# Kernel optimization log

Measured on AMD Instinct MI355X. Metric: run time of the kernel, lower is better.

## Reference

```python
import jax, jax.numpy as jnp
import numpy as np

EPS = 1e-8

def rms_norm(x, scale):
    # full RMSNorm over last dim (p < 0 branch): norm/sqrt(d)
    d = x.shape[-1]
    norm = jnp.linalg.norm(x, ord=2, axis=-1, keepdims=True)
    rms = norm * (d ** -0.5)
    return scale * (x / (rms + EPS))

def setup_inputs() -> dict:
    key = jax.random.key(0)
    ks = jax.random.split(key, 4)
    B, N, C, H = 2, 2048, 1024, 16
    hd = C // H
    x = jax.random.normal(ks[0], (B, N, C), dtype=jnp.float32)
    Wqkv = jax.random.normal(ks[1], (C, 3 * C), dtype=jnp.float32) * (C ** -0.5)
    Wproj = jax.random.normal(ks[2], (C, C), dtype=jnp.float32) * (C ** -0.5)
    bproj = jnp.zeros((C,), dtype=jnp.float32)
    q_scale = jnp.ones((hd,), dtype=jnp.float32)
    k_scale = jnp.ones((hd,), dtype=jnp.float32)
    return {"x": x, "Wqkv": Wqkv, "Wproj": Wproj, "bproj": bproj,
            "q_scale": q_scale, "k_scale": k_scale}

def reference(x, Wqkv, Wproj, bproj, q_scale, k_scale):
    B, N, C = x.shape
    H = 16
    hd = C // H
    scale = hd ** -0.5
    qkv = (x @ Wqkv).reshape(B, N, 3, H, hd)
    qkv = jnp.transpose(qkv, (2, 0, 3, 1, 4))  # t b h n c
    q, k, v = qkv[0], qkv[1], qkv[2]
    q = rms_norm(q, q_scale)
    k = rms_norm(k, k_scale)
    attn = jnp.einsum('bhnc,bhmc->bhnm', q, k) * scale
    attn = jax.nn.softmax(attn, axis=-1)
    out = jnp.einsum('bhnm,bhmc->bhnc', attn, v)
    out = jnp.transpose(out, (0, 2, 1, 3)).reshape(B, N, C)
    return out @ Wproj + bproj
```

## Files before the change

kernel.cpp:

```cpp
#include <hip/hip_runtime.h>


typedef _Float16 half_t;
typedef __attribute__((ext_vector_type(2))) __fp16 fp16x2;
typedef __attribute__((ext_vector_type(4))) _Float16 half4v;
typedef __attribute__((ext_vector_type(8))) _Float16 half8;
typedef __attribute__((ext_vector_type(4))) float f32x4;
typedef __attribute__((ext_vector_type(4))) unsigned uint4v;

#define DI __device__ __forceinline__

DI void gl_lds16(const void* g, void* l) {
    __builtin_amdgcn_global_load_lds((const __attribute__((address_space(1))) void*)g,
                                     (__attribute__((address_space(3))) void*)l, 16, 0, 0);
}

DI float exp2_fast(float x) {
    float r;
    asm("v_exp_f32 %0, %1" : "=v"(r) : "v"(x));
    return r;
}

DI void pl32_swap(unsigned& a, unsigned& b) {
    asm("v_permlane32_swap_b32 %0, %1" : "+v"(a), "+v"(b));
}
DI void pl16_swap(unsigned& a, unsigned& b) {
    asm("v_permlane16_swap_b32 %0, %1" : "+v"(a), "+v"(b));
}

DI unsigned pk_u32(float lo, float hi) {
    fp16x2 t = __builtin_amdgcn_cvt_pkrtz(lo, hi);
    return *(unsigned*)&t;
}

__global__ void prep_all(const float* __restrict__ x, const float* __restrict__ Wqkv,
                         const float* __restrict__ Wproj, half_t* __restrict__ xh,
                         half_t* __restrict__ wqt, half_t* __restrict__ wpt) {
    __shared__ float t[32][33];
    int bid = blockIdx.x;
    if (bid < 4096) {
        int i = (bid * 256 + threadIdx.x) * 4;
        float4 v = *(const float4*)(x + i);
        half4v o;
        o[0] = (half_t)v.x; o[1] = (half_t)v.y; o[2] = (half_t)v.z; o[3] = (half_t)v.w;
        *(half4v*)(xh + i) = o;
    } else if (bid < 4096 + 3072) {
        int i = bid - 4096;
        int c0 = (i % 96) * 32, r0 = (i / 96) * 32;
        int tx = threadIdx.x & 31, ty = threadIdx.x >> 5;
#pragma unroll
        for (int k = 0; k < 4; k++)
            t[ty + 8 * k][tx] = Wqkv[(size_t)(r0 + ty + 8 * k) * 3072 + c0 + tx];
        __syncthreads();
#pragma unroll
        for (int k = 0; k < 4; k++)
            wqt[(size_t)(c0 + ty + 8 * k) * 1024 + r0 + tx] = (half_t)t[tx][ty + 8 * k];
    } else {
        int i = bid - 4096 - 3072;
        int c0 = (i % 32) * 32, r0 = (i / 32) * 32;
        int tx = threadIdx.x & 31, ty = threadIdx.x >> 5;
#pragma unroll
        for (int k = 0; k < 4; k++)
            t[ty + 8 * k][tx] = Wproj[(size_t)(r0 + ty + 8 * k) * 1024 + c0 + tx];
        __syncthreads();
#pragma unroll
        for (int k = 0; k < 4; k++)
            wpt[(size_t)(c0 + ty + 8 * k) * 1024 + r0 + tx] = (half_t)t[tx][ty + 8 * k];
    }
}

__global__ __launch_bounds__(256) void gemm_qkv(
    const half_t* __restrict__ A, const half_t* __restrict__ Bt,
    const float* __restrict__ qs, const float* __restrict__ ks,
    half_t* __restrict__ qh, half_t* __restrict__ kh, half_t* __restrict__ vth) {
    const int K = 1024;
    __shared__ __align__(16) half_t Al[2][128 * 64];
    __shared__ __align__(16) half_t Bl[2][128 * 64];
    int tid = threadIdx.x;
    int w = tid >> 6, l = tid & 63;
    int wr = w >> 1, wc = w & 1;
    int g = l >> 4, r = l & 15;
    int m0 = blockIdx.x * 128, n0 = blockIdx.y * 128;
    f32x4 acc[4][4] = {};

#define STAGE_QKV(kt, buf)                                                        \
    {                                                                             \
        _Pragma("unroll")                                                         \
        for (int p = 0; p < 4; p++) {                                             \
            int ci = p * 256 + tid;                                               \
            int row = ci >> 3, c = ci & 7, lc = c ^ (row & 7);                    \
            gl_lds16(A + (size_t)(m0 + row) * K + (kt) * 64 + lc * 8,             \
                     &Al[buf][0] + ci * 8);                                       \
            gl_lds16(Bt + (size_t)(n0 + row) * K + (kt) * 64 + lc * 8,            \
                     &Bl[buf][0] + ci * 8);                                       \
        }                                                                         \
    }

    STAGE_QKV(0, 0);
    __syncthreads();
    int cur = 0;
    for (int kt = 0; kt < 16; kt++) {
        if (kt < 15) STAGE_QKV(kt + 1, cur ^ 1);
#pragma unroll
        for (int ks2 = 0; ks2 < 2; ks2++) {
            half8 af[4], bf[4];
#pragma unroll
            for (int i = 0; i < 4; i++) {
                int row = wr * 64 + i * 16 + r;
                af[i] = *(const half8*)(&Al[cur][0] + row * 64 + (((4 * ks2 + g) ^ (row & 7)) << 3));
                int rowb = wc * 64 + i * 16 + r;
                bf[i] = *(const half8*)(&Bl[cur][0] + rowb * 64 + (((4 * ks2 + g) ^ (rowb & 7)) << 3));
            }
#pragma unroll
            for (int i = 0; i < 4; i++)
#pragma unroll
                for (int j = 0; j < 4; j++)
                    acc[i][j] = __builtin_amdgcn_mfma_f32_16x16x32_f16(af[i], bf[j], acc[i][j], 0, 0, 0);
        }
        __syncthreads();
        cur ^= 1;
    }

    int tsec = n0 >> 10;
    if (tsec == 2) {
#pragma unroll
        for (int i = 0; i < 4; i++)
#pragma unroll
            for (int j = 0; j < 4; j++) {
                int gcol = n0 + wc * 64 + j * 16 + r;
                int h = (gcol >> 6) & 15;
                int f = gcol & 63;
                int growb = m0 + wr * 64 + i * 16 + g * 4;
                int b = growb >> 11;
                int n = growb & 2047;
                half4v pv;
#pragma unroll
                for (int rr = 0; rr < 4; rr++) pv[rr] = (half_t)acc[i][j][rr];
                *(half4v*)(vth + ((size_t)(b * 16 + h) * 64 + f) * 2048 + n) = pv;
            }
    } else {
        const float* sc = (tsec == 0) ? qs : ks;
        half_t* dst = (tsec == 0) ? qh : kh;
        float extra = (tsec == 0) ? (0.125f * 1.44269504f) : 1.0f;
        float scv[4];
#pragma unroll
        for (int j = 0; j < 4; j++) scv[j] = sc[j * 16 + r];
#pragma unroll
        for (int i = 0; i < 4; i++)
#pragma unroll
            for (int rr = 0; rr < 4; rr++) {
                float ss = 0.f;
#pragma unroll
                for (int j = 0; j < 4; j++) ss += acc[i][j][rr] * acc[i][j][rr];
#pragma unroll
                for (int d = 1; d < 16; d <<= 1) ss += __shfl_xor(ss, d, 64);
                float inv = extra / (sqrtf(ss) * 0.125f + 1e-8f);
                int grow = m0 + wr * 64 + i * 16 + g * 4 + rr;
                int b = grow >> 11;
                int n = grow & 2047;
#pragma unroll
                for (int j = 0; j < 4; j++) {
                    int gcol = n0 + wc * 64 + j * 16 + r;
                    int h = (gcol >> 6) & 15;
                    int f = gcol & 63;
                    dst[((size_t)(b * 16 + h) * 2048 + n) * 64 + f] =
                        (half_t)(acc[i][j][rr] * inv * scv[j]);
                }
            }
    }
}

__global__ __launch_bounds__(512, 6) void attn(
    const half_t* __restrict__ qh, const half_t* __restrict__ kh,
    const half_t* __restrict__ vth, half_t* __restrict__ aoh) {
    int bh = blockIdx.y;
    int q0 = blockIdx.x * 128;
    const half_t* Qp = qh + (size_t)bh * 2048 * 64;
    const half_t* Kp = kh + (size_t)bh * 2048 * 64;
    const half_t* Vp = vth + (size_t)bh * 64 * 2048;
    __shared__ __align__(16) half_t Kl[2][64 * 64];
    __shared__ __align__(16) half_t Vl[2][64 * 64];
    int tid = threadIdx.x, w = tid >> 6, l = tid & 63, g = l >> 4, r = l & 15;

    int srow = tid >> 3, sc = tid & 7, slc = sc ^ (srow & 7);
    const half_t* kst = Kp + (size_t)srow * 64 + slc * 8;
    const half_t* vst = Vp + (size_t)srow * 2048 + slc * 8;

    int koff[8], voff[8];
#pragma unroll
    for (int ks = 0; ks < 2; ks++)
#pragma unroll
        for (int tt = 0; tt < 4; tt++) {
            int row = tt * 16 + r;
            koff[ks * 4 + tt] = row * 64 + (((4 * ks + g) ^ (row & 7)) << 3);
        }
#pragma unroll
    for (int ks2 = 0; ks2 < 2; ks2++)
#pragma unroll
        for (int cf = 0; cf < 4; cf++) {
            int row = cf * 16 + r;
            voff[ks2 * 4 + cf] = row * 64 + (((4 * ks2 + g) ^ (row & 7)) << 3);
        }

    half8 qf[2];
#pragma unroll
    for (int ks = 0; ks < 2; ks++)
        qf[ks] = *(const half8*)(Qp + (size_t)(q0 + w * 16 + r) * 64 + ks * 32 + g * 8);

    f32x4 o[4] = {};
    float m = -1e30f, lsum = 0.f;

    gl_lds16(kst, &Kl[0][0] + tid * 8);
    gl_lds16(vst, &Vl[0][0] + tid * 8);
    __syncthreads();

#define ATTN_TILE(BUF, T)                                                          \
    {                                                                              \
        if ((T) < 31) {                                                            \
            gl_lds16(kst + ((T) + 1) * 4096, &Kl[(BUF) ^ 1][0] + tid * 8);         \
            gl_lds16(vst + ((T) + 1) * 64, &Vl[(BUF) ^ 1][0] + tid * 8);           \
        }                                                                          \
        const half_t* Kc = &Kl[BUF][0];                                            \
        const half_t* Vc = &Vl[BUF][0];                                            \
        f32x4 s[4] = {};                                                           \
        _Pragma("unroll")                                                          \
        for (int ks = 0; ks < 2; ks++)                                             \
            _Pragma("unroll")                                                      \
            for (int tt = 0; tt < 4; tt++) {                                       \
                half8 kf = *(const half8*)(Kc + koff[ks * 4 + tt]);                \
                s[tt] = __builtin_amdgcn_mfma_f32_16x16x32_f16(kf, qf[ks], s[tt], 0, 0, 0); \
            }                                                                      \
        float thr = m + 11.0f;                                                     \
        bool ok = true;                                                            \
        _Pragma("unroll")                                                          \
        for (int tt = 0; tt < 4; tt++)                                             \
            _Pragma("unroll")                                                      \
            for (int e = 0; e < 4; e++) ok = ok && (s[tt][e] <= thr);              \
        if (!__all(ok)) {                                                          \
            float mx = -1e30f;                                                     \
            _Pragma("unroll")                                                      \
            for (int tt = 0; tt < 4; tt++)                                         \
                mx = fmaxf(mx, fmaxf(fmaxf(s[tt][0], s[tt][1]), fmaxf(s[tt][2], s[tt][3]))); \
            mx = fmaxf(mx, __shfl_xor(mx, 16, 64));                                \
            mx = fmaxf(mx, __shfl_xor(mx, 32, 64));                                \
            float mn = fmaxf(m, mx);                                               \
            float fac = exp2_fast(m - mn);                                         \
            lsum *= fac;                                                           \
            _Pragma("unroll")                                                      \
            for (int cf = 0; cf < 4; cf++) {                                       \
                o[cf][0] *= fac; o[cf][1] *= fac; o[cf][2] *= fac; o[cf][3] *= fac; \
            }                                                                      \
            m = mn;                                                                \
        }                                                                          \
        _Pragma("unroll")                                                          \
        for (int tt = 0; tt < 4; tt++)                                             \
            _Pragma("unroll")                                                      \
            for (int e = 0; e < 4; e++) {                                          \
                float p = exp2_fast(s[tt][e] - m);                                 \
                s[tt][e] = p;                                                      \
                lsum += p;                                                         \
            }                                                                      \
        unsigned W[4][2];                                                          \
        _Pragma("unroll")                                                          \
        for (int tt = 0; tt < 4; tt++) {                                           \
            W[tt][0] = pk_u32(s[tt][0], s[tt][1]);                                 \
            W[tt][1] = pk_u32(s[tt][2], s[tt][3]);                                 \
        }                                                                          \
        _Pragma("unroll")                                                          \
        for (int ks2 = 0; ks2 < 2; ks2++) {                                        \
            unsigned b0 = W[2 * ks2][0], b2 = W[2 * ks2 + 1][0];                   \
            unsigned b1 = W[2 * ks2][1], b3 = W[2 * ks2 + 1][1];                   \
            pl32_swap(b0, b2); pl16_swap(b0, b2);                                  \
            pl32_swap(b1, b3); pl16_swap(b1, b3);                                  \
            uint4v pw; pw[0] = b0; pw[1] = b1; pw[2] = b2; pw[3] = b3;             \
            half8 pf = *(half8*)&pw;                                               \
            _Pragma("unroll")                                                      \
            for (int cf = 0; cf < 4; cf++) {                                       \
                half8 vf = *(const half8*)(Vc + voff[ks2 * 4 + cf]);               \
                o[cf] = __builtin_amdgcn_mfma_f32_16x16x32_f16(vf, pf, o[cf], 0, 0, 0); \
            }                                                                      \
        }                                                                          \
        __syncthreads();                                                           \
    }

    for (int t = 0; t < 32; t += 2) {
        ATTN_TILE(0, t);
        ATTN_TILE(1, t + 1);
    }

    lsum += __shfl_xor(lsum, 16, 64);
    lsum += __shfl_xor(lsum, 32, 64);

    int b = bh >> 4, h = bh & 15;
    int n = q0 + w * 16 + r;
    float inv = 1.0f / lsum;
#pragma unroll
    for (int cf = 0; cf < 4; cf++) {
        half4v ov;
#pragma unroll
        for (int reg = 0; reg < 4; reg++) ov[reg] = (half_t)(o[cf][reg] * inv);
        *(half4v*)(aoh + ((size_t)b * 2048 + n) * 1024 + h * 64 + cf * 16 + g * 4) = ov;
    }
}

__global__ __launch_bounds__(256) void gemm_proj(
    const half_t* __restrict__ A, const half_t* __restrict__ Bt,
    const float* __restrict__ bias, float* __restrict__ out) {
    const int K = 1024;
    __shared__ __align__(16) half_t Al[128 * 64];
    __shared__ __align__(16) half_t Bl[128 * 64];
    int tid = threadIdx.x, w = tid >> 6, l = tid & 63;
    int wr = w >> 1, wc = w & 1, g = l >> 4, r = l & 15;
    int m0 = blockIdx.x * 128, n0 = blockIdx.y * 128;
    f32x4 acc[4][4] = {};

    for (int k0 = 0; k0 < K; k0 += 64) {
#pragma unroll
        for (int p = 0; p < 4; p++) {
            int ci = (p * 4 + w) * 64 + l;
            int row = ci >> 3, c = ci & 7;
            int lc = c ^ (row & 7);
            gl_lds16(A + (size_t)(m0 + row) * K + k0 + lc * 8, Al + (p * 4 + w) * 512);
            gl_lds16(Bt + (size_t)(n0 + row) * K + k0 + lc * 8, Bl + (p * 4 + w) * 512);
        }
        __syncthreads();
#pragma unroll
        for (int ks = 0; ks < 2; ks++) {
            half8 af[4], bf[4];
#pragma unroll
            for (int i = 0; i < 4; i++) {
                int row = wr * 64 + i * 16 + r;
                af[i] = *(const half8*)(Al + row * 64 + (((4 * ks + g) ^ (row & 7)) << 3));
                int rowb = wc * 64 + i * 16 + r;
                bf[i] = *(const half8*)(Bl + rowb * 64 + (((4 * ks + g) ^ (rowb & 7)) << 3));
            }
#pragma unroll
            for (int i = 0; i < 4; i++)
#pragma unroll
                for (int j = 0; j < 4; j++)
                    acc[i][j] = __builtin_amdgcn_mfma_f32_16x16x32_f16(af[i], bf[j], acc[i][j], 0, 0, 0);
        }
        __syncthreads();
    }

#pragma unroll
    for (int i = 0; i < 4; i++)
#pragma unroll
        for (int j = 0; j < 4; j++) {
            int gcol = n0 + wc * 64 + j * 16 + r;
            float bv = bias[gcol];
#pragma unroll
            for (int rr = 0; rr < 4; rr++) {
                int grow = m0 + wr * 64 + i * 16 + g * 4 + rr;
                out[(size_t)grow * 1024 + gcol] = acc[i][j][rr] + bv;
            }
        }
}

extern "C" void kernel_launch(void* const* d_in, const int* in_sizes, int n_in,
                              void* d_out, int out_size, void* d_ws, size_t ws_size,
                              hipStream_t stream) {
    const float* x = (const float*)d_in[0];
    const float* Wqkv = (const float*)d_in[1];
    const float* Wproj = (const float*)d_in[2];
    const float* bproj = (const float*)d_in[3];
    const float* qscale = (const float*)d_in[4];
    const float* kscale = (const float*)d_in[5];
    float* out = (float*)d_out;

    char* ws = (char*)d_ws;
    half_t* xh  = (half_t*)(ws + 0);
    half_t* wqt = (half_t*)(ws + 8388608);
    half_t* wpt = (half_t*)(ws + 14680064);
    half_t* qh  = (half_t*)(ws + 16777216);
    half_t* kh  = (half_t*)(ws + 25165824);
    half_t* vth = (half_t*)(ws + 33554432);
    half_t* aoh = (half_t*)(ws + 41943040);

    prep_all<<<8192, 256, 0, stream>>>(x, Wqkv, Wproj, xh, wqt, wpt);
    gemm_qkv<<<dim3(32, 24), 256, 0, stream>>>(xh, wqt, qscale, kscale, qh, kh, vth);
    attn<<<dim3(16, 32), 512, 0, stream>>>(qh, kh, vth, aoh);
    gemm_proj<<<dim3(32, 8), 256, 0, stream>>>(aoh, wpt, bproj, out);
}
```

Measured before the change: 131.6 us.

## Split attention over key dimension into two halves with a combine kernel

Splits each attention block's 2048-key loop into two independent halves via a third grid dimension, doubling the grid from 512 to 1024 blocks to improve occupancy across the GPU's compute units. Each half writes a normalized fp16 partial output plus its running max and sum, and a new combine kernel merges them with exp2-weighted rescaling. This adds an extra kernel launch and an extra round trip of partial outputs through memory, and stores intermediate results in fp16. Workspace buffers are rearranged so the partials reuse the region that held the converted input and QKV weights.

```diff
diff --git a/kernel.cpp b/kernel.cpp
--- a/kernel.cpp
+++ b/kernel.cpp
@@ -170,14 +170,15 @@
     }
 }
 
-__global__ __launch_bounds__(512, 6) void attn(
+__global__ __launch_bounds__(512, 8) void attn(
     const half_t* __restrict__ qh, const half_t* __restrict__ kh,
-    const half_t* __restrict__ vth, half_t* __restrict__ aoh) {
-    int bh = blockIdx.y;
+    const half_t* __restrict__ vth, half_t* __restrict__ po16,
+    float2* __restrict__ pml) {
+    int bh = blockIdx.y, hf = blockIdx.z;
     int q0 = blockIdx.x * 128;
     const half_t* Qp = qh + (size_t)bh * 2048 * 64;
-    const half_t* Kp = kh + (size_t)bh * 2048 * 64;
-    const half_t* Vp = vth + (size_t)bh * 64 * 2048;
+    const half_t* Kp = kh + (size_t)bh * 2048 * 64 + (size_t)hf * 1024 * 64;
+    const half_t* Vp = vth + (size_t)bh * 64 * 2048 + hf * 1024;
     __shared__ __align__(16) half_t Kl[2][64 * 64];
     __shared__ __align__(16) half_t Vl[2][64 * 64];
     int tid = threadIdx.x, w = tid >> 6, l = tid & 63, g = l >> 4, r = l & 15;
@@ -216,7 +217,7 @@
 
 #define ATTN_TILE(BUF, T)                                                          \
     {                                                                              \
-        if ((T) < 31) {                                                            \
+        if ((T) < 15) {                                                            \
             gl_lds16(kst + ((T) + 1) * 4096, &Kl[(BUF) ^ 1][0] + tid * 8);         \
             gl_lds16(vst + ((T) + 1) * 64, &Vl[(BUF) ^ 1][0] + tid * 8);           \
         }                                                                          \
@@ -283,7 +284,7 @@
         __syncthreads();                                                           \
     }
 
-    for (int t = 0; t < 32; t += 2) {
+    for (int t = 0; t < 16; t += 2) {
         ATTN_TILE(0, t);
         ATTN_TILE(1, t + 1);
     }
@@ -291,16 +292,40 @@
     lsum += __shfl_xor(lsum, 16, 64);
     lsum += __shfl_xor(lsum, 32, 64);
 
-    int b = bh >> 4, h = bh & 15;
     int n = q0 + w * 16 + r;
+    size_t pq = (size_t)(hf * 32 + bh) * 2048 + n;
     float inv = 1.0f / lsum;
 #pragma unroll
     for (int cf = 0; cf < 4; cf++) {
         half4v ov;
 #pragma unroll
         for (int reg = 0; reg < 4; reg++) ov[reg] = (half_t)(o[cf][reg] * inv);
-        *(half4v*)(aoh + ((size_t)b * 2048 + n) * 1024 + h * 64 + cf * 16 + g * 4) = ov;
-    }
+        *(half4v*)(po16 + pq * 64 + cf * 16 + g * 4) = ov;
+    }
+    if (l < 16) pml[pq] = make_float2(m, lsum);
+}
+
+__global__ void attn_combine(const half_t* __restrict__ po16,
+                             const float2* __restrict__ pml,
+                             half_t* __restrict__ aoh) {
+    int idx = blockIdx.x * 256 + threadIdx.x;
+    int d4 = idx & 15;
+    int q = (idx >> 4) & 2047;
+    int bh = idx >> 15;
+    float2 ml0 = pml[(size_t)bh * 2048 + q];
+    float2 ml1 = pml[(size_t)(32 + bh) * 2048 + q];
+    float M = fmaxf(ml0.x, ml1.x);
+    float w0 = exp2_fast(ml0.x - M) * ml0.y;
+    float w1 = exp2_fast(ml1.x - M) * ml1.y;
+    float inv = 1.0f / (w0 + w1);
+    w0 *= inv; w1 *= inv;
+    half4v a = *(const half4v*)(po16 + ((size_t)bh * 2048 + q) * 64 + d4 * 4);
+    half4v b2 = *(const half4v*)(po16 + ((size_t)(32 + bh) * 2048 + q) * 64 + d4 * 4);
+    half4v o;
+#pragma unroll
+    for (int e = 0; e < 4; e++) o[e] = (half_t)((float)a[e] * w0 + (float)b2[e] * w1);
+    int b = bh >> 4, h = bh & 15;
+    *(half4v*)(aoh + ((size_t)b * 2048 + q) * 1024 + h * 64 + d4 * 4) = o;
 }
 
 __global__ __launch_bounds__(256) void gemm_proj(
@@ -369,16 +394,19 @@
     float* out = (float*)d_out;
 
     char* ws = (char*)d_ws;
-    half_t* xh  = (half_t*)(ws + 0);
-    half_t* wqt = (half_t*)(ws + 8388608);
-    half_t* wpt = (half_t*)(ws + 14680064);
-    half_t* qh  = (half_t*)(ws + 16777216);
-    half_t* kh  = (half_t*)(ws + 25165824);
-    half_t* vth = (half_t*)(ws + 33554432);
-    half_t* aoh = (half_t*)(ws + 41943040);
+    half_t* xh   = (half_t*)(ws + 0);
+    half_t* wqt  = (half_t*)(ws + 8388608);
+    half_t* po16 = (half_t*)(ws + 0);
+    float2* pml  = (float2*)(ws + 16777216);
+    half_t* qh   = (half_t*)(ws + 17825792);
+    half_t* kh   = (half_t*)(ws + 26214400);
+    half_t* vth  = (half_t*)(ws + 34603008);
+    half_t* wpt  = (half_t*)(ws + 42991616);
+    half_t* aoh  = (half_t*)(ws + 45088768);
 
     prep_all<<<8192, 256, 0, stream>>>(x, Wqkv, Wproj, xh, wqt, wpt);
     gemm_qkv<<<dim3(32, 24), 256, 0, stream>>>(xh, wqt, qscale, kscale, qh, kh, vth);
-    attn<<<dim3(16, 32), 512, 0, stream>>>(qh, kh, vth, aoh);
+    attn<<<dim3(16, 32, 2), 512, 0, stream>>>(qh, kh, vth, po16, pml);
+    attn_combine<<<4096, 256, 0, stream>>>(po16, pml, aoh);
     gemm_proj<<<dim3(32, 8), 256, 0, stream>>>(aoh, wpt, bproj, out);
 }
```

New measurement: 184.3 us. 1.4x slower.

## Split attention KV range across two wave groups and merge partial softmax

Applied to the files above, without the earlier changes.

The attention kernel now handles 64 queries per block instead of 128. The 8 waves split into two halves, and each half processes one half of the key/value sequence with 32-key tiles. At the end, the partial outputs and their max/sum statistics are combined through shared memory with a log-sum-exp merge. This doubles the grid to 1024 blocks and raises the occupancy hint, aiming at better CU utilization and latency hiding. The cost is extra LDS traffic, a merge step in which half the waves sit idle, and smaller MFMA batches per tile.

```diff
diff --git a/kernel.cpp b/kernel.cpp
--- a/kernel.cpp
+++ b/kernel.cpp
@@ -170,77 +170,78 @@
     }
 }
 
-__global__ __launch_bounds__(512, 6) void attn(
+__global__ __launch_bounds__(512, 8) void attn(
     const half_t* __restrict__ qh, const half_t* __restrict__ kh,
     const half_t* __restrict__ vth, half_t* __restrict__ aoh) {
     int bh = blockIdx.y;
-    int q0 = blockIdx.x * 128;
+    int q0 = blockIdx.x * 64;
+    int tid = threadIdx.x, w = tid >> 6, l = tid & 63, g = l >> 4, r = l & 15;
+    int hf = w >> 2, qs = w & 3, lt = tid & 255;
+
     const half_t* Qp = qh + (size_t)bh * 2048 * 64;
-    const half_t* Kp = kh + (size_t)bh * 2048 * 64;
-    const half_t* Vp = vth + (size_t)bh * 64 * 2048;
-    __shared__ __align__(16) half_t Kl[2][64 * 64];
-    __shared__ __align__(16) half_t Vl[2][64 * 64];
-    int tid = threadIdx.x, w = tid >> 6, l = tid & 63, g = l >> 4, r = l & 15;
-
-    int srow = tid >> 3, sc = tid & 7, slc = sc ^ (srow & 7);
-    const half_t* kst = Kp + (size_t)srow * 64 + slc * 8;
-    const half_t* vst = Vp + (size_t)srow * 2048 + slc * 8;
-
-    int koff[8], voff[8];
+    const half_t* Kp = kh + (size_t)bh * 2048 * 64 + (size_t)hf * 1024 * 64;
+    const half_t* Vp = vth + (size_t)bh * 64 * 2048 + hf * 1024;
+
+    __shared__ __align__(16) char smem[32768];
+    half_t* Kb[2] = {(half_t*)(smem + hf * 8192), (half_t*)(smem + hf * 8192 + 4096)};
+    half_t* Vb[2] = {(half_t*)(smem + 16384 + hf * 8192), (half_t*)(smem + 16384 + hf * 8192 + 4096)};
+
+    int krow = lt >> 3, kc = lt & 7, klc = kc ^ (krow & 7);
+    const half_t* kst = Kp + (size_t)krow * 64 + klc * 8;
+    int vrow = lt >> 2, vc = lt & 3, vlc = vc ^ ((vrow >> 1) & 3);
+    const half_t* vst = Vp + (size_t)vrow * 2048 + vlc * 8;
+
+    int koff[4], voff[4];
 #pragma unroll
     for (int ks = 0; ks < 2; ks++)
 #pragma unroll
-        for (int tt = 0; tt < 4; tt++) {
+        for (int tt = 0; tt < 2; tt++) {
             int row = tt * 16 + r;
-            koff[ks * 4 + tt] = row * 64 + (((4 * ks + g) ^ (row & 7)) << 3);
-        }
-#pragma unroll
-    for (int ks2 = 0; ks2 < 2; ks2++)
-#pragma unroll
-        for (int cf = 0; cf < 4; cf++) {
-            int row = cf * 16 + r;
-            voff[ks2 * 4 + cf] = row * 64 + (((4 * ks2 + g) ^ (row & 7)) << 3);
-        }
+            koff[ks * 2 + tt] = row * 64 + (((ks * 4 + g) ^ (row & 7)) << 3);
+        }
+#pragma unroll
+    for (int cf = 0; cf < 4; cf++) {
+        int row = cf * 16 + r;
+        voff[cf] = row * 32 + ((g ^ ((row >> 1) & 3)) << 3);
+    }
 
     half8 qf[2];
 #pragma unroll
     for (int ks = 0; ks < 2; ks++)
-        qf[ks] = *(const half8*)(Qp + (size_t)(q0 + w * 16 + r) * 64 + ks * 32 + g * 8);
+        qf[ks] = *(const half8*)(Qp + (size_t)(q0 + qs * 16 + r) * 64 + ks * 32 + g * 8);
 
     f32x4 o[4] = {};
     float m = -1e30f, lsum = 0.f;
 
-    gl_lds16(kst, &Kl[0][0] + tid * 8);
-    gl_lds16(vst, &Vl[0][0] + tid * 8);
+    gl_lds16(kst, Kb[0] + lt * 8);
+    gl_lds16(vst, Vb[0] + lt * 8);
     __syncthreads();
 
 #define ATTN_TILE(BUF, T)                                                          \
     {                                                                              \
         if ((T) < 31) {                                                            \
-            gl_lds16(kst + ((T) + 1) * 4096, &Kl[(BUF) ^ 1][0] + tid * 8);         \
-            gl_lds16(vst + ((T) + 1) * 64, &Vl[(BUF) ^ 1][0] + tid * 8);           \
+            gl_lds16(kst + ((T) + 1) * 2048, Kb[(BUF) ^ 1] + lt * 8);              \
+            gl_lds16(vst + ((T) + 1) * 32, Vb[(BUF) ^ 1] + lt * 8);                \
         }                                                                          \
-        const half_t* Kc = &Kl[BUF][0];                                            \
-        const half_t* Vc = &Vl[BUF][0];                                            \
-        f32x4 s[4] = {};                                                           \
+        const half_t* Kc = Kb[BUF];                                                \
+        const half_t* Vc = Vb[BUF];                                                \
+        f32x4 s[2] = {};                                                           \
         _Pragma("unroll")                                                          \
         for (int ks = 0; ks < 2; ks++)                                             \
             _Pragma("unroll")                                                      \
-            for (int tt = 0; tt < 4; tt++) {                                       \
-                half8 kf = *(const half8*)(Kc + koff[ks * 4 + tt]);                \
+            for (int tt = 0; tt < 2; tt++) {                                       \
+                half8 kf = *(const half8*)(Kc + koff[ks * 2 + tt]);                \
                 s[tt] = __builtin_amdgcn_mfma_f32_16x16x32_f16(kf, qf[ks], s[tt], 0, 0, 0); \
             }                                                                      \
         float thr = m + 11.0f;                                                     \
         bool ok = true;                                                            \
         _Pragma("unroll")                                                          \
-        for (int tt = 0; tt < 4; tt++)                                             \
+        for (int tt = 0; tt < 2; tt++)                                             \
             _Pragma("unroll")                                                      \
             for (int e = 0; e < 4; e++) ok = ok && (s[tt][e] <= thr);              \
         if (!__all(ok)) {                                                          \
-            float mx = -1e30f;                                                     \
-            _Pragma("unroll")                                                      \
-            for (int tt = 0; tt < 4; tt++)                                         \
-                mx = fmaxf(mx, fmaxf(fmaxf(s[tt][0], s[tt][1]), fmaxf(s[tt][2], s[tt][3]))); \
+            float mx = fmaxf(fmaxf(s[0][0], s[0][1]), fmaxf(s[0][2], s[0][3]));    \
+            mx = fmaxf(mx, fmaxf(fmaxf(s[1][0], s[1][1]), fmaxf(s[1][2], s[1][3]))); \
             mx = fmaxf(mx, __shfl_xor(mx, 16, 64));                                \
             mx = fmaxf(mx, __shfl_xor(mx, 32, 64));                                \
             float mn = fmaxf(m, mx);                                               \
@@ -253,32 +254,25 @@
             m = mn;                                                                \
         }                                                                          \
         _Pragma("unroll")                                                          \
-        for (int tt = 0; tt < 4; tt++)                                             \
+        for (int tt = 0; tt < 2; tt++)                                             \
             _Pragma("unroll")                                                      \
             for (int e = 0; e < 4; e++) {                                          \
                 float p = exp2_fast(s[tt][e] - m);                                 \
                 s[tt][e] = p;                                                      \
                 lsum += p;                                                         \
             }                                                                      \
-        unsigned W[4][2];                                                          \
+        unsigned b0 = pk_u32(s[0][0], s[0][1]);                                    \
+        unsigned b1 = pk_u32(s[0][2], s[0][3]);                                    \
+        unsigned b2 = pk_u32(s[1][0], s[1][1]);                                    \
+        unsigned b3 = pk_u32(s[1][2], s[1][3]);                                    \
+        pl32_swap(b0, b2); pl16_swap(b0, b2);                                      \
+        pl32_swap(b1, b3); pl16_swap(b1, b3);                                      \
+        uint4v pw; pw[0] = b0; pw[1] = b1; pw[2] = b2; pw[3] = b3;                 \
+        half8 pf = *(half8*)&pw;                                                   \
         _Pragma("unroll")                                                          \
-        for (int tt = 0; tt < 4; tt++) {                                           \
-            W[tt][0] = pk_u32(s[tt][0], s[tt][1]);                                 \
-            W[tt][1] = pk_u32(s[tt][2], s[tt][3]);                                 \
-        }                                                                          \
-        _Pragma("unroll")                                                          \
-        for (int ks2 = 0; ks2 < 2; ks2++) {                                        \
-            unsigned b0 = W[2 * ks2][0], b2 = W[2 * ks2 + 1][0];                   \
-            unsigned b1 = W[2 * ks2][1], b3 = W[2 * ks2 + 1][1];                   \
-            pl32_swap(b0, b2); pl16_swap(b0, b2);                                  \
-            pl32_swap(b1, b3); pl16_swap(b1, b3);                                  \
-            uint4v pw; pw[0] = b0; pw[1] = b1; pw[2] = b2; pw[3] = b3;             \
-            half8 pf = *(half8*)&pw;                                               \
-            _Pragma("unroll")                                                      \
-            for (int cf = 0; cf < 4; cf++) {                                       \
-                half8 vf = *(const half8*)(Vc + voff[ks2 * 4 + cf]);               \
-                o[cf] = __builtin_amdgcn_mfma_f32_16x16x32_f16(vf, pf, o[cf], 0, 0, 0); \
-            }                                                                      \
+        for (int cf = 0; cf < 4; cf++) {                                           \
+            half8 vf = *(const half8*)(Vc + voff[cf]);                             \
+            o[cf] = __builtin_amdgcn_mfma_f32_16x16x32_f16(vf, pf, o[cf], 0, 0, 0); \
         }                                                                          \
         __syncthreads();                                                           \
     }
@@ -291,15 +285,35 @@
     lsum += __shfl_xor(lsum, 16, 64);
     lsum += __shfl_xor(lsum, 32, 64);
 
-    int b = bh >> 4, h = bh & 15;
-    int n = q0 + w * 16 + r;
-    float inv = 1.0f / lsum;
-#pragma unroll
-    for (int cf = 0; cf < 4; cf++) {
-        half4v ov;
-#pragma unroll
-        for (int reg = 0; reg < 4; reg++) ov[reg] = (half_t)(o[cf][reg] * inv);
-        *(half4v*)(aoh + ((size_t)b * 2048 + n) * 1024 + h * 64 + cf * 16 + g * 4) = ov;
+    float* mo = (float*)smem;
+    float* mml = (float*)(smem + 17408);
+    int q2 = qs * 16 + r;
+    if (hf) {
+#pragma unroll
+        for (int cf = 0; cf < 4; cf++)
+            *(f32x4*)(mo + q2 * 68 + cf * 16 + g * 4) = o[cf];
+        if (l < 16) {
+            mml[q2 * 2] = m;
+            mml[q2 * 2 + 1] = lsum;
+        }
+    }
+    __syncthreads();
+    if (!hf) {
+        float m1 = mml[q2 * 2], ls1 = mml[q2 * 2 + 1];
+        float M = fmaxf(m, m1);
+        float w0 = exp2_fast(m - M), w1 = exp2_fast(m1 - M);
+        float inv = 1.0f / (w0 * lsum + w1 * ls1);
+        w0 *= inv; w1 *= inv;
+        int n = q0 + q2;
+        int b = bh >> 4, h = bh & 15;
+#pragma unroll
+        for (int cf = 0; cf < 4; cf++) {
+            f32x4 o1 = *(const f32x4*)(mo + q2 * 68 + cf * 16 + g * 4);
+            half4v ov;
+#pragma unroll
+            for (int e = 0; e < 4; e++) ov[e] = (half_t)(o[cf][e] * w0 + o1[e] * w1);
+            *(half4v*)(aoh + ((size_t)b * 2048 + n) * 1024 + h * 64 + cf * 16 + g * 4) = ov;
+        }
     }
 }
 
@@ -379,6 +393,6 @@
 
     prep_all<<<8192, 256, 0, stream>>>(x, Wqkv, Wproj, xh, wqt, wpt);
     gemm_qkv<<<dim3(32, 24), 256, 0, stream>>>(xh, wqt, qscale, kscale, qh, kh, vth);
-    attn<<<dim3(16, 32), 512, 0, stream>>>(qh, kh, vth, aoh);
+    attn<<<dim3(32, 32), 512, 0, stream>>>(qh, kh, vth, aoh);
     gemm_proj<<<dim3(32, 8), 256, 0, stream>>>(aoh, wpt, bproj, out);
 }
```

After: 133.9 us. About the same (+1.7%).
